# Kernel optimization log

Measured on AMD Instinct MI355X. Metric: run time of the kernel, lower is better.

Reference implementation:

```python
import jax, jax.numpy as jnp
import numpy as np

B = 128   # molecules
A = 64    # atoms per molecule
N = B * A # 8192 atoms
K = 32    # neighbors per atom
P = N * K # 262144 pairs
D = 256   # hidden dim of the modeled atomwise energy net


def setup_inputs() -> dict:
    key = jax.random.key(0)
    ks = jax.random.split(key, 8)
    xyz = jax.random.normal(ks[0], (N, 3), dtype=jnp.float32)
    r_ij = jax.random.normal(ks[1], (P, 3), dtype=jnp.float32)
    nbrs0 = jnp.repeat(jnp.arange(N, dtype=jnp.int64), K)           # center atom of each pair
    nbrs1 = jax.random.randint(ks[2], (P,), 0, N, dtype=jnp.int64)  # neighbor atom
    nbrs = jnp.stack([nbrs0, nbrs1], axis=1)
    # well-conditioned per-molecule lattices, stacked as [3*B, 3] like batch['cell']
    cell = jnp.tile(10.0 * jnp.eye(3, dtype=jnp.float32), (B, 1)) + 0.1 * jax.random.normal(ks[3], (3 * B, 3), dtype=jnp.float32)
    W_self = 0.1 * jax.random.normal(ks[4], (3, D), dtype=jnp.float32)
    W_pair = 0.1 * jax.random.normal(ks[5], (3, D), dtype=jnp.float32)
    w1 = 0.1 * jax.random.normal(ks[6], (D,), dtype=jnp.float32)
    w2 = 0.1 * jax.random.normal(ks[7], (D,), dtype=jnp.float32)
    return dict(xyz=xyz, r_ij=r_ij, nbrs=nbrs, cell=cell, W_self=W_self, W_pair=W_pair, w1=w1, w2=w2)


def reference(xyz, r_ij, nbrs, cell, W_self, W_pair, w1, w2):
    # mol_idx = arange(B).repeat_interleave(num_atoms) with num_atoms = A for all molecules
    mol_idx = jnp.repeat(jnp.arange(B), A)
    nbrs0 = nbrs[:, 0]

    def energy_fn(xyz_, rij_):
        # modeled atomwise energy network (upstream of SumPool)
        e_self = jnp.tanh(xyz_ @ W_self) @ w1                       # [N]
        phi = jnp.tanh(rij_ @ W_pair) @ w2                          # [P]
        e_atom = e_self + jax.ops.segment_sum(phi, nbrs0, num_segments=N)
        # SumPool: scatter_add over mol_idx (mean=False)
        return jax.ops.segment_sum(e_atom, mol_idx, num_segments=B)  # [B]

    energy = energy_fn(xyz, r_ij)

    # grad of total pooled energy w.r.t. xyz (energy_grad) and r_ij (for stress)
    g_xyz, g_rij = jax.grad(lambda x, r: energy_fn(x, r).sum(), argnums=(0, 1))(xyz, r_ij)

    # stress: per-atom 3x3 = sum_{p: nbrs[p,0]==i} outer(dE/dr_ij[p], r_ij[p]),
    # then summed per molecule — replaces the original per-atom Python loop
    outer = g_rij[:, :, None] * r_ij[:, None, :]                    # [P,3,3]
    atom_stress = jax.ops.segment_sum(outer, nbrs0, num_segments=N) # [N,3,3]
    mol_stress = jax.ops.segment_sum(atom_stress, mol_idx, num_segments=B)  # [B,3,3]

    cells = cell.reshape(B, 3, 3)
    volume = jnp.abs(jnp.linalg.det(cells))                         # [B]
    stress = (mol_stress / volume[:, None, None]).reshape(B * 3, 3) # flatten(start_dim=0, end_dim=1)

    return energy, g_xyz, stress
```

## Files before the change

### kernel.cpp

```cpp
#include <hip/hip_runtime.h>

#define NB 128
#define NN 8192
#define NP 262144
#define ND 256
#define PAIR_BLOCKS 512
#define ATOM_BLOCKS 32

#define C2   2.885390081777927f
#define INVC 0.3465735902799726f

__device__ __forceinline__ float exp2_fast(float x) {
#if __has_builtin(__builtin_amdgcn_exp2f)
    return __builtin_amdgcn_exp2f(x);
#else
    float r; asm("v_exp_f32 %0, %1" : "=v"(r) : "v"(x)); return r;
#endif
}
__device__ __forceinline__ float rcp_fast(float x) {
#if __has_builtin(__builtin_amdgcn_rcpf)
    return __builtin_amdgcn_rcpf(x);
#else
    float r; asm("v_rcp_f32 %0, %1" : "=v"(r) : "v"(x)); return r;
#endif
}

__device__ __forceinline__ float tanh_from_scaled(float hp) {
    float t = rcp_fast(exp2_fast(hp) + 1.f);
    return fmaf(-2.f, t, 1.f);
}

__global__ __launch_bounds__(256) void fused_kernel(
    const float* __restrict__ xyz,
    const float* __restrict__ r_ij,
    const float* __restrict__ W_self,
    const float* __restrict__ W_pair,
    const float* __restrict__ w1,
    const float* __restrict__ w2,
    float* __restrict__ g_xyz,
    float* __restrict__ ws_e,
    float* __restrict__ ws_s)
{
    __shared__ float4 Wq[ND];
    const int tid = threadIdx.x;
    const bool is_pair = blockIdx.x < PAIR_BLOCKS;
    {
        const float* W  = is_pair ? W_pair : W_self;
        const float* wv = is_pair ? w2 : w1;
        Wq[tid] = make_float4(C2 * W[tid], C2 * W[ND + tid], C2 * W[2 * ND + tid], wv[tid]);
    }
    __syncthreads();

    if (is_pair) {
        const int base = blockIdx.x * 512;
        const int p0 = base + tid, p1 = base + 256 + tid;
        const float a0 = r_ij[3 * p0], a1 = r_ij[3 * p0 + 1], a2 = r_ij[3 * p0 + 2];
        const float b0 = r_ij[3 * p1], b1 = r_ij[3 * p1 + 1], b2 = r_ij[3 * p1 + 2];
        float phA = 0.f, gA0 = 0.f, gA1 = 0.f, gA2 = 0.f;
        float phB = 0.f, gB0 = 0.f, gB1 = 0.f, gB2 = 0.f;
        #pragma unroll 4
        for (int d = 0; d < ND; ++d) {
            float4 w = Wq[d];
            float hA = fmaf(a0, w.x, fmaf(a1, w.y, a2 * w.z));
            float uA = tanh_from_scaled(hA);
            phA = fmaf(uA, w.w, phA);
            float sA = w.w * fmaf(-uA, uA, 1.f);
            gA0 = fmaf(sA, w.x, gA0); gA1 = fmaf(sA, w.y, gA1); gA2 = fmaf(sA, w.z, gA2);
            float hB = fmaf(b0, w.x, fmaf(b1, w.y, b2 * w.z));
            float uB = tanh_from_scaled(hB);
            phB = fmaf(uB, w.w, phB);
            float sB = w.w * fmaf(-uB, uB, 1.f);
            gB0 = fmaf(sB, w.x, gB0); gB1 = fmaf(sB, w.y, gB1); gB2 = fmaf(sB, w.z, gB2);
        }
        gA0 *= INVC; gA1 *= INVC; gA2 *= INVC;
        gB0 *= INVC; gB1 *= INVC; gB2 *= INVC;

        float v[10];
        v[0] = phA + phB;
        v[1] = fmaf(gA0, a0, gB0 * b0); v[2] = fmaf(gA0, a1, gB0 * b1); v[3] = fmaf(gA0, a2, gB0 * b2);
        v[4] = fmaf(gA1, a0, gB1 * b0); v[5] = fmaf(gA1, a1, gB1 * b1); v[6] = fmaf(gA1, a2, gB1 * b2);
        v[7] = fmaf(gA2, a0, gB2 * b0); v[8] = fmaf(gA2, a1, gB2 * b1); v[9] = fmaf(gA2, a2, gB2 * b2);

        #pragma unroll
        for (int off = 32; off > 0; off >>= 1)
            #pragma unroll
            for (int k = 0; k < 10; ++k) v[k] += __shfl_down(v[k], off);

        if ((tid & 63) == 0) {
            const int b = blockIdx.x >> 2;
            atomicAdd(&ws_e[b], v[0]);
            #pragma unroll
            for (int k = 0; k < 9; ++k) atomicAdd(&ws_s[b * 9 + k], v[k + 1]);
        }
    } else {
        const int i = (blockIdx.x - PAIR_BLOCKS) * 256 + tid;
        const float x0 = xyz[3 * i], x1 = xyz[3 * i + 1], x2 = xyz[3 * i + 2];
        float e = 0.f, g0 = 0.f, g1 = 0.f, g2 = 0.f;
        #pragma unroll 4
        for (int d = 0; d < ND; ++d) {
            float4 w = Wq[d];
            float h = fmaf(x0, w.x, fmaf(x1, w.y, x2 * w.z));
            float t = tanh_from_scaled(h);
            e = fmaf(t, w.w, e);
            float s = w.w * fmaf(-t, t, 1.f);
            g0 = fmaf(s, w.x, g0); g1 = fmaf(s, w.y, g1); g2 = fmaf(s, w.z, g2);
        }
        g_xyz[3 * i]     = g0 * INVC;
        g_xyz[3 * i + 1] = g1 * INVC;
        g_xyz[3 * i + 2] = g2 * INVC;
        #pragma unroll
        for (int off = 32; off > 0; off >>= 1) e += __shfl_down(e, off);
        if ((tid & 63) == 0) atomicAdd(&ws_e[i >> 6], e);
    }
}

__global__ void finalize_kernel(
    const float* __restrict__ cell,
    const float* __restrict__ ws_e,
    const float* __restrict__ ws_s,
    float* __restrict__ energy,
    float* __restrict__ stress)
{
    const int b = threadIdx.x;
    if (b >= NB) return;
    energy[b] = ws_e[b];
    const float* c = cell + 9 * b;
    float det = c[0] * (c[4] * c[8] - c[5] * c[7])
              - c[1] * (c[3] * c[8] - c[5] * c[6])
              + c[2] * (c[3] * c[7] - c[4] * c[6]);
    float inv = rcp_fast(fabsf(det));
    #pragma unroll
    for (int k = 0; k < 9; ++k)
        stress[b * 9 + k] = ws_s[b * 9 + k] * inv;
}

extern "C" void kernel_launch(void* const* d_in, const int* in_sizes, int n_in,
                              void* d_out, int out_size, void* d_ws, size_t ws_size,
                              hipStream_t stream) {
    const float* xyz    = (const float*)d_in[0];
    const float* r_ij   = (const float*)d_in[1];
    const float* cell   = (const float*)d_in[3];
    const float* W_self = (const float*)d_in[4];
    const float* W_pair = (const float*)d_in[5];
    const float* w1     = (const float*)d_in[6];
    const float* w2     = (const float*)d_in[7];

    float* out    = (float*)d_out;
    float* energy = out;
    float* g_xyz  = out + NB;
    float* stress = out + NB + NN * 3;
    float* ws_e   = (float*)d_ws;
    float* ws_s   = ws_e + NB;

    hipMemsetAsync(d_ws, 0, (NB + NB * 9) * sizeof(float), stream);
    fused_kernel<<<PAIR_BLOCKS + ATOM_BLOCKS, 256, 0, stream>>>(
        xyz, r_ij, W_self, W_pair, w1, w2, g_xyz, ws_e, ws_s);
    finalize_kernel<<<1, 128, 0, stream>>>(cell, ws_e, ws_s, energy, stress);
}
```

Measured before the change: 49.78 us.

## Merge atom work into every pair block, splitting each atom across 16 lanes

```diff
diff --git a/kernel.cpp b/kernel.cpp
--- a/kernel.cpp
+++ b/kernel.cpp
@@ -4,8 +4,10 @@
 #define NN 8192
 #define NP 262144
 #define ND 256
-#define PAIR_BLOCKS 512
-#define ATOM_BLOCKS 32
+
+#define NBLOCKS 512
+#define PAIRS_PER_BLOCK 512
+#define ATOMS_PER_BLOCK 16
 
 #define C2   2.885390081777927f
 #define INVC 0.3465735902799726f
@@ -37,30 +39,32 @@
     const float* __restrict__ W_pair,
     const float* __restrict__ w1,
     const float* __restrict__ w2,
+    float* __restrict__ energy,
     float* __restrict__ g_xyz,
-    float* __restrict__ ws_e,
-    float* __restrict__ ws_s)
+    float* __restrict__ stress)
 {
-    __shared__ float4 Wq[ND];
+    __shared__ float4 Wp[ND];
+    __shared__ float4 Ws[ND];
     const int tid = threadIdx.x;
-    const bool is_pair = blockIdx.x < PAIR_BLOCKS;
-    {
-        const float* W  = is_pair ? W_pair : W_self;
-        const float* wv = is_pair ? w2 : w1;
-        Wq[tid] = make_float4(C2 * W[tid], C2 * W[ND + tid], C2 * W[2 * ND + tid], wv[tid]);
-    }
+    const int bx  = blockIdx.x;
+    const int mol = bx >> 2;
+
+    Wp[tid] = make_float4(C2 * W_pair[tid], C2 * W_pair[ND + tid],
+                          C2 * W_pair[2 * ND + tid], w2[tid]);
+    Ws[tid] = make_float4(C2 * W_self[tid], C2 * W_self[ND + tid],
+                          C2 * W_self[2 * ND + tid], w1[tid]);
     __syncthreads();
 
-    if (is_pair) {
-        const int base = blockIdx.x * 512;
-        const int p0 = base + tid, p1 = base + 256 + tid;
+    {
+        const int p0 = bx * PAIRS_PER_BLOCK + tid;
+        const int p1 = p0 + 256;
         const float a0 = r_ij[3 * p0], a1 = r_ij[3 * p0 + 1], a2 = r_ij[3 * p0 + 2];
         const float b0 = r_ij[3 * p1], b1 = r_ij[3 * p1 + 1], b2 = r_ij[3 * p1 + 2];
         float phA = 0.f, gA0 = 0.f, gA1 = 0.f, gA2 = 0.f;
         float phB = 0.f, gB0 = 0.f, gB1 = 0.f, gB2 = 0.f;
         #pragma unroll 4
         for (int d = 0; d < ND; ++d) {
-            float4 w = Wq[d];
+            float4 w = Wp[d];
             float hA = fmaf(a0, w.x, fmaf(a1, w.y, a2 * w.z));
             float uA = tanh_from_scaled(hA);
             phA = fmaf(uA, w.w, phA);
@@ -87,51 +91,59 @@
             for (int k = 0; k < 10; ++k) v[k] += __shfl_down(v[k], off);
 
         if ((tid & 63) == 0) {
-            const int b = blockIdx.x >> 2;
-            atomicAdd(&ws_e[b], v[0]);
+            atomicAdd(&energy[mol], v[0]);
             #pragma unroll
-            for (int k = 0; k < 9; ++k) atomicAdd(&ws_s[b * 9 + k], v[k + 1]);
+            for (int k = 0; k < 9; ++k)
+                atomicAdd(&stress[mol * 9 + k], v[k + 1]);
         }
-    } else {
-        const int i = (blockIdx.x - PAIR_BLOCKS) * 256 + tid;
-        const float x0 = xyz[3 * i], x1 = xyz[3 * i + 1], x2 = xyz[3 * i + 2];
+    }
+
+    {
+        const int atom  = bx * ATOMS_PER_BLOCK + (tid >> 4);
+        const int slice = tid & 15;
+        const float x0 = xyz[3 * atom], x1 = xyz[3 * atom + 1], x2 = xyz[3 * atom + 2];
         float e = 0.f, g0 = 0.f, g1 = 0.f, g2 = 0.f;
-        #pragma unroll 4
-        for (int d = 0; d < ND; ++d) {
-            float4 w = Wq[d];
+        #pragma unroll
+        for (int k = 0; k < 16; ++k) {
+            float4 w = Ws[slice + 16 * k];
             float h = fmaf(x0, w.x, fmaf(x1, w.y, x2 * w.z));
-            float t = tanh_from_scaled(h);
-            e = fmaf(t, w.w, e);
-            float s = w.w * fmaf(-t, t, 1.f);
+            float u = tanh_from_scaled(h);
+            e = fmaf(u, w.w, e);
+            float s = w.w * fmaf(-u, u, 1.f);
             g0 = fmaf(s, w.x, g0); g1 = fmaf(s, w.y, g1); g2 = fmaf(s, w.z, g2);
         }
-        g_xyz[3 * i]     = g0 * INVC;
-        g_xyz[3 * i + 1] = g1 * INVC;
-        g_xyz[3 * i + 2] = g2 * INVC;
         #pragma unroll
-        for (int off = 32; off > 0; off >>= 1) e += __shfl_down(e, off);
-        if ((tid & 63) == 0) atomicAdd(&ws_e[i >> 6], e);
+        for (int off = 8; off > 0; off >>= 1) {
+            e  += __shfl_down(e, off);
+            g0 += __shfl_down(g0, off);
+            g1 += __shfl_down(g1, off);
+            g2 += __shfl_down(g2, off);
+        }
+        if (slice == 0) {
+            g_xyz[3 * atom]     = g0 * INVC;
+            g_xyz[3 * atom + 1] = g1 * INVC;
+            g_xyz[3 * atom + 2] = g2 * INVC;
+        }
+        e += __shfl_down(e, 32);
+        e += __shfl_down(e, 16);
+        if ((tid & 63) == 0) atomicAdd(&energy[mol], e);
     }
 }
 
 __global__ void finalize_kernel(
     const float* __restrict__ cell,
-    const float* __restrict__ ws_e,
-    const float* __restrict__ ws_s,
-    float* __restrict__ energy,
     float* __restrict__ stress)
 {
     const int b = threadIdx.x;
     if (b >= NB) return;
-    energy[b] = ws_e[b];
     const float* c = cell + 9 * b;
     float det = c[0] * (c[4] * c[8] - c[5] * c[7])
               - c[1] * (c[3] * c[8] - c[5] * c[6])
               + c[2] * (c[3] * c[7] - c[4] * c[6]);
-    float inv = rcp_fast(fabsf(det));
+    float inv = 1.f / fabsf(det);
     #pragma unroll
     for (int k = 0; k < 9; ++k)
-        stress[b * 9 + k] = ws_s[b * 9 + k] * inv;
+        stress[b * 9 + k] *= inv;
 }
 
 extern "C" void kernel_launch(void* const* d_in, const int* in_sizes, int n_in,
@@ -149,11 +161,11 @@
     float* energy = out;
     float* g_xyz  = out + NB;
     float* stress = out + NB + NN * 3;
-    float* ws_e   = (float*)d_ws;
-    float* ws_s   = ws_e + NB;
 
-    hipMemsetAsync(d_ws, 0, (NB + NB * 9) * sizeof(float), stream);
-    fused_kernel<<<PAIR_BLOCKS + ATOM_BLOCKS, 256, 0, stream>>>(
-        xyz, r_ij, W_self, W_pair, w1, w2, g_xyz, ws_e, ws_s);
-    finalize_kernel<<<1, 128, 0, stream>>>(cell, ws_e, ws_s, energy, stress);
+    hipMemsetAsync(energy, 0, NB * sizeof(float), stream);
+    hipMemsetAsync(stress, 0, NB * 9 * sizeof(float), stream);
+
+    fused_kernel<<<NBLOCKS, 256, 0, stream>>>(
+        xyz, r_ij, W_self, W_pair, w1, w2, energy, g_xyz, stress);
+    finalize_kernel<<<1, 128, 0, stream>>>(cell, stress);
 }
```

Result: slower. 63.35 us (+27.2%).
